# Kernel tuning notes

Measured on AMD Instinct MI355X. Metric: run time of the kernel, lower is better.

The kernel has to match this reference:

```python
import jax, jax.numpy as jnp
import numpy as np

NUM_HEADS = 16


def setup_inputs() -> dict:
    key = jax.random.key(0)
    ks = jax.random.split(key, 6)
    B, N, L, C = 2, 1024, 4096, 1024
    x_obj = jax.random.normal(ks[0], (B, N, C), dtype=jnp.float32)
    x_ctx = jax.random.normal(ks[1], (B, L, C), dtype=jnp.float32)
    s = 1.0 / np.sqrt(C)
    Wq = jax.random.normal(ks[2], (C, C), dtype=jnp.float32) * s
    Wkv = jax.random.normal(ks[3], (C, 2 * C), dtype=jnp.float32) * s
    Wproj = jax.random.normal(ks[4], (C, C), dtype=jnp.float32) * s
    bproj = jax.random.normal(ks[5], (C,), dtype=jnp.float32) * 0.01
    return {"x_obj": x_obj, "x_ctx": x_ctx, "Wq": Wq, "Wkv": Wkv,
            "Wproj": Wproj, "bproj": bproj}


def _split_heads(t, H):
    # [B, T, C] -> [B, H, T, d]
    B, T, C = t.shape
    return t.reshape(B, T, H, C // H).transpose(0, 2, 1, 3)


def reference(x_obj, x_ctx, Wq, Wkv, Wproj, bproj):
    B, N, C = x_obj.shape
    H = NUM_HEADS
    d = C // H
    scale = d ** -0.5

    q = _split_heads(x_obj @ Wq, H)                      # [B,H,N,d]

    kv_o = x_obj @ Wkv                                   # [B,N,2C] -> (2,H,d) split
    k_obj = _split_heads(kv_o[..., :C], H)               # [B,H,N,d]
    v_obj = _split_heads(kv_o[..., C:], H)

    kv_c = x_ctx @ Wkv                                   # [B,L,2C]
    k_ctx = _split_heads(kv_c[..., :C], H)               # [B,H,L,d]
    v_ctx = _split_heads(kv_c[..., C:], H)

    k = jnp.concatenate([k_obj, k_ctx], axis=2)          # [B,H,N+L,d]
    v = jnp.concatenate([v_obj, v_ctx], axis=2)

    attn = jnp.einsum('bhnd,bhmd->bhnm', q, k) * scale   # [B,H,N,N+L]
    attn = jax.nn.softmax(attn, axis=-1)
    out = jnp.einsum('bhnm,bhmd->bhnd', attn, v)         # [B,H,N,d]
    out = out.transpose(0, 2, 1, 3).reshape(B, N, C)
    return out @ Wproj + bproj
```

## Files before the change

### kernel.cpp

```cpp
#include <hip/hip_runtime.h>
#include <stdint.h>

typedef unsigned short u16;
typedef unsigned int   u32;
typedef __attribute__((ext_vector_type(8))) short bf16x8;
typedef __attribute__((ext_vector_type(4))) float f32x4;

__device__ __forceinline__ u16 f2bf(float f) {
    union { float f; u32 u; } v; v.f = f;
    return (u16)((v.u + 0x7FFFu + ((v.u >> 16) & 1u)) >> 16);
}
__device__ __forceinline__ float bf2f(u16 h) {
    union { u32 u; float f; } v; v.u = ((u32)h) << 16; return v.f;
}
__device__ __forceinline__ u32 fbits(float f) {
    union { float f; u32 u; } v; v.f = f; return v.u;
}

__device__ __forceinline__ void async16(const u16* g, u16* l) {
    typedef __attribute__((address_space(1))) const u32 gq;
    typedef __attribute__((address_space(3))) u32 lq;
    __builtin_amdgcn_global_load_lds((gq*)g, (lq*)l, 16, 0, 0);
}

__global__ void cvt_all_k(const float* __restrict__ xo, const float* __restrict__ xc,
                          u16* __restrict__ Xc,
                          const float* __restrict__ Wq, const float* __restrict__ Wkv,
                          const float* __restrict__ Wp,
                          u16* __restrict__ Wqt, u16* __restrict__ Wkt,
                          u16* __restrict__ Wpt)
{
    __shared__ __align__(16) u16 Ts[64][72];
    int id = blockIdx.x, t = threadIdx.x;
    if (id < 10240) {
        int row = id, cid = t * 4;
        int b = row >= 5120, s = row - b * 5120;
        const float* src = (s < 1024)
            ? xo + ((size_t)(b * 1024 + s)) * 1024 + cid
            : xc + ((size_t)(b * 4096 + s - 1024)) * 1024 + cid;
        float4 f = *(const float4*)src;
        union { u16 a[4]; uint2 v; } p;
        p.a[0]=f2bf(f.x); p.a[1]=f2bf(f.y); p.a[2]=f2bf(f.z); p.a[3]=f2bf(f.w);
        *(uint2*)(Xc + (size_t)row * 1024 + cid) = p.v;
        return;
    }
    int wid = id - 10240;
    const float* W; u16* Wt; int N, tile;
    if (wid < 256)      { W = Wq;  Wt = Wqt; N = 1024; tile = wid; }
    else if (wid < 768) { W = Wkv; Wt = Wkt; N = 2048; tile = wid - 256; }
    else                { W = Wp;  Wt = Wpt; N = 1024; tile = wid - 768; }
    int nt = N >> 6;
    int n0 = (tile % nt) * 64, k0 = (tile / nt) * 64;
    int lr = t >> 2, lc = (t & 3) * 16;
    const float* src = W + (size_t)(k0 + lr) * N + n0 + lc;
    union { u16 a[8]; uint4 v; } p0, p1;
    float4 f0 = *(const float4*)(src),      f1 = *(const float4*)(src + 4);
    float4 f2 = *(const float4*)(src + 8),  f3 = *(const float4*)(src + 12);
    p0.a[0]=f2bf(f0.x); p0.a[1]=f2bf(f0.y); p0.a[2]=f2bf(f0.z); p0.a[3]=f2bf(f0.w);
    p0.a[4]=f2bf(f1.x); p0.a[5]=f2bf(f1.y); p0.a[6]=f2bf(f1.z); p0.a[7]=f2bf(f1.w);
    p1.a[0]=f2bf(f2.x); p1.a[1]=f2bf(f2.y); p1.a[2]=f2bf(f2.z); p1.a[3]=f2bf(f2.w);
    p1.a[4]=f2bf(f3.x); p1.a[5]=f2bf(f3.y); p1.a[6]=f2bf(f3.z); p1.a[7]=f2bf(f3.w);
    *(uint4*)&Ts[lr][lc]     = p0.v;
    *(uint4*)&Ts[lr][lc + 8] = p1.v;
    __syncthreads();
    union { u16 a[8]; uint4 v; } q0, q1;
#pragma unroll
    for (int j = 0; j < 8; ++j) q0.a[j] = Ts[lc + j][lr];
#pragma unroll
    for (int j = 0; j < 8; ++j) q1.a[j] = Ts[lc + 8 + j][lr];
    u16* dst = Wt + (size_t)(n0 + lr) * 1024 + k0 + lc;
    *(uint4*)dst       = q0.v;
    *(uint4*)(dst + 8) = q1.v;
}

__global__ __launch_bounds__(256, 2)
void gemm_qkv(const u16* __restrict__ A, const u16* __restrict__ Wqt,
              const u16* __restrict__ Wkt, u16* __restrict__ q,
              u16* __restrict__ Kh, u16* __restrict__ Vh)
{
    __shared__ __align__(16) u16 smem[17408];
    u16* As = smem;
    u16* Bs = smem + 4096;

    const int t = threadIdx.x, w = t >> 6;
    const int lane = t & 63, quad = lane >> 4, l16 = lane & 15;
    const int id = blockIdx.x;
    const bool qm = id >= 1280;
    int m0, n0; const u16* Bt;
    if (qm) { int t2 = id - 1280; m0 = (t2 >> 3) * 128; n0 = (t2 & 7) * 128; Bt = Wqt; }
    else    { m0 = (id >> 4) * 128; n0 = (id & 15) * 128; Bt = Wkt; }
    const int wr = (w >> 1) * 64, wc = (w & 1) * 64;

    const int sr0 = w * 32 + (lane >> 2), sr1 = sr0 + 16;
    const int cg  = (lane & 3) ^ ((lane >> 4) & 3);
    u16* abase = As + w * 1024;
    u16* bbase = Bs + w * 1024;

    const u16 *ar0, *ar1;
    {
        int g0 = m0 + sr0, g1 = m0 + sr1;
        if (qm) {
            ar0 = A + ((size_t)(g0 >> 10) * 5120 + (g0 & 1023)) * 1024;
            ar1 = A + ((size_t)(g1 >> 10) * 5120 + (g1 & 1023)) * 1024;
        } else {
            ar0 = A + (size_t)g0 * 1024;
            ar1 = A + (size_t)g1 * 1024;
        }
        ar0 += cg * 8; ar1 += cg * 8;
    }
    const u16* br0 = Bt + (size_t)(n0 + sr0) * 1024 + cg * 8;
    const u16* br1 = Bt + (size_t)(n0 + sr1) * 1024 + cg * 8;

    f32x4 acc[4][4] = {};
    const int sel = (quad ^ (l16 >> 2)) * 8;

    for (int k0 = 0; k0 < 1024; k0 += 32) {
        async16(ar0 + k0, abase);
        async16(ar1 + k0, abase + 512);
        async16(br0 + k0, bbase);
        async16(br1 + k0, bbase + 512);
        __syncthreads();

        bf16x8 av[4], bv[4];
#pragma unroll
        for (int i = 0; i < 4; ++i)
            av[i] = *(const bf16x8*)&As[(wr + i * 16 + l16) * 32 + sel];
#pragma unroll
        for (int j = 0; j < 4; ++j)
            bv[j] = *(const bf16x8*)&Bs[(wc + j * 16 + l16) * 32 + sel];
#pragma unroll
        for (int i = 0; i < 4; ++i)
#pragma unroll
            for (int j = 0; j < 4; ++j)
                acc[i][j] = __builtin_amdgcn_mfma_f32_16x16x32_bf16(av[i], bv[j], acc[i][j], 0, 0, 0);
        __syncthreads();
    }

    if (qm) {
        const float SC = 0.180336880f;
#pragma unroll
        for (int j = 0; j < 4; ++j) {
            int col = n0 + wc + j * 16 + l16;
#pragma unroll
            for (int i = 0; i < 4; ++i) {
                int rowb = m0 + wr + i * 16 + quad * 4;
#pragma unroll
                for (int r = 0; r < 4; ++r)
                    q[(size_t)(rowb + r) * 1024 + col] = f2bf(acc[i][j][r] * SC);
            }
        }
        return;
    }
    int b = m0 >= 5120;
    int keyb = m0 - b * 5120;
    if (n0 < 1024) {
#pragma unroll
        for (int j = 0; j < 4; ++j) {
            int col = n0 + wc + j * 16 + l16;
#pragma unroll
            for (int i = 0; i < 4; ++i) {
                int rowb = m0 + wr + i * 16 + quad * 4;
                int key = rowb - b * 5120;
                int bh = b * 16 + (col >> 6), d = col & 63;
                u16* dst = Kh + ((size_t)bh * 5120 + key) * 64 + d;
#pragma unroll
                for (int r = 0; r < 4; ++r) dst[r * 64] = f2bf(acc[i][j][r]);
            }
        }
    } else {
        u16* T = smem;
#pragma unroll
        for (int j = 0; j < 4; ++j) {
            int d2 = wc + j * 16 + l16;
#pragma unroll
            for (int i = 0; i < 4; ++i) {
                int kl = wr + i * 16 + quad * 4;
                union { u16 a[4]; uint2 v; } pk;
#pragma unroll
                for (int r = 0; r < 4; ++r) pk.a[r] = f2bf(acc[i][j][r]);
                *(uint2*)&T[d2 * 136 + kl] = pk.v;
            }
        }
        __syncthreads();
        int hb = (n0 - 1024) >> 6;
#pragma unroll
        for (int p = 0; p < 8; ++p) {
            int idx = p * 256 + t;
            int d2 = idx >> 4, k0c = (idx & 15) * 8;
            uint4 vv = *(const uint4*)&T[d2 * 136 + k0c];
            int bh = b * 16 + hb + (d2 >> 6), d = d2 & 63;
            *(uint4*)(Vh + ((size_t)bh * 64 + d) * 5120 + keyb + k0c) = vv;
        }
    }
}

__global__ __launch_bounds__(256, 2)
void gemm_proj(const u16* __restrict__ A, const u16* __restrict__ Bt,
               const float* __restrict__ bias, float* __restrict__ Cf)
{
    __shared__ __align__(16) u16 As[128 * 32];
    __shared__ __align__(16) u16 Bs[64 * 32];

    const int t = threadIdx.x, w = t >> 6;
    const int lane = t & 63, quad = lane >> 4, l16 = lane & 15;
    const int m0 = blockIdx.y * 128, n0 = blockIdx.x * 64;
    const int wr = w * 32;

    const int sr0 = w * 32 + (lane >> 2), sr1 = sr0 + 16;
    const int cg  = (lane & 3) ^ ((lane >> 4) & 3);
    u16* abase = As + w * 1024;
    u16* bbase = Bs + w * 512;

    const u16* ar0 = A + (size_t)(m0 + sr0) * 1024 + cg * 8;
    const u16* ar1 = A + (size_t)(m0 + sr1) * 1024 + cg * 8;
    const u16* br0 = Bt + (size_t)(n0 + w * 16 + (lane >> 2)) * 1024 + cg * 8;

    f32x4 acc[2][4] = {};
    const int sel = (quad ^ (l16 >> 2)) * 8;

    for (int k0 = 0; k0 < 1024; k0 += 32) {
        async16(ar0 + k0, abase);
        async16(ar1 + k0, abase + 512);
        async16(br0 + k0, bbase);
        __syncthreads();

        bf16x8 av[2], bv[4];
#pragma unroll
        for (int i = 0; i < 2; ++i)
            av[i] = *(const bf16x8*)&As[(wr + i * 16 + l16) * 32 + sel];
#pragma unroll
        for (int j = 0; j < 4; ++j)
            bv[j] = *(const bf16x8*)&Bs[(j * 16 + l16) * 32 + sel];
#pragma unroll
        for (int i = 0; i < 2; ++i)
#pragma unroll
            for (int j = 0; j < 4; ++j)
                acc[i][j] = __builtin_amdgcn_mfma_f32_16x16x32_bf16(av[i], bv[j], acc[i][j], 0, 0, 0);
        __syncthreads();
    }

#pragma unroll
    for (int j = 0; j < 4; ++j) {
        int col = n0 + j * 16 + l16;
        float bvl = bias[col];
#pragma unroll
        for (int i = 0; i < 2; ++i) {
            int rowb = m0 + wr + i * 16 + quad * 4;
#pragma unroll
            for (int r = 0; r < 4; ++r)
                Cf[(size_t)(rowb + r) * 1024 + col] = acc[i][j][r] + bvl;
        }
    }
}

__global__ __launch_bounds__(256, 4)
void attn_k(const u16* __restrict__ Q, const u16* __restrict__ Kh,
            const u16* __restrict__ Vh, u16* __restrict__ Op,
            float* __restrict__ Lp)
{
    __shared__ __align__(16) u16 Ks[2][4096];
    __shared__ __align__(16) u16 Vt[4096];
    __shared__ __align__(16) u16 Ps[4096];

    const int tid  = threadIdx.x;
    const int wave = tid >> 6, lane = tid & 63;
    const int quad = lane >> 4, l16 = lane & 15;
    const int bx = blockIdx.x;
    const int x   = bx & 7;
    const int seq = bx >> 3;
    const int qt  = seq & 7;
    const int kg  = seq >> 3;
    const int g   = x + 8 * kg;
    const int part = g >> 5;
    const int bh   = g & 31;
    const int h = bh & 15, b = bh >> 4;

    const int qrow0 = b * 1024 + qt * 128 + wave * 32;
    const u16* qbase = Q + (size_t)qrow0 * 1024 + h * 64;

    bf16x8 aq[2][2];
#pragma unroll
    for (int rt = 0; rt < 2; ++rt) {
        aq[rt][0] = *(const bf16x8*)(qbase + (size_t)(rt * 16 + l16) * 1024 +      quad * 8);
        aq[rt][1] = *(const bf16x8*)(qbase + (size_t)(rt * 16 + l16) * 1024 + 32 + quad * 8);
    }

    union { u32 u[4]; bf16x8 v; } onesf;
#pragma unroll
    for (int i = 0; i < 4; ++i) onesf.u[i] = 0x3F803F80u;

    f32x4 o[2][4] = {};
    f32x4 lacc[2] = {};

    const u16* kbase = Kh + (size_t)bh * 5120 * 64;
    const u16* vbase = Vh + (size_t)bh * 64 * 5120;
    const int srow = tid >> 2;
    const int scg  = (tid & 3) * 2;
    const int m7   = srow & 7;
    const int l7   = l16 & 7;
    u16* vdst0 = Vt + srow * 64 + ((scg ^ m7) * 8);
    u16* vdst1 = Vt + srow * 64 + (((scg + 1) ^ m7) * 8);
    u16* psw   = Ps + wave * 1024;
    const int m_beg = part * 1024;

    const int keyA = tid >> 3;
    const int chA  = (tid & 7) ^ (keyA & 7);
    const u16* kga = kbase + (size_t)(m_beg + keyA) * 64 + chA * 8;
    u16* klds = &Ks[0][0] + wave * 512;

    const u16* vptr = vbase + (size_t)srow * 5120 + m_beg + (tid & 3) * 4;

    async16(kga,        klds);
    async16(kga + 2048, klds + 2048);
    uint2 vg0 = *(const uint2*)(vptr);
    uint2 vg1 = *(const uint2*)(vptr + 16);
    uint2 vg2 = *(const uint2*)(vptr + 32);
    uint2 vg3 = *(const uint2*)(vptr + 48);

    for (int c = 0; c < 16; ++c) {
        {
            uint4 o0, o1;
            o0.x = __builtin_amdgcn_perm(vg1.x, vg0.x, 0x05040100u);
            o0.y = __builtin_amdgcn_perm(vg3.x, vg2.x, 0x05040100u);
            o0.z = __builtin_amdgcn_perm(vg1.x, vg0.x, 0x07060302u);
            o0.w = __builtin_amdgcn_perm(vg3.x, vg2.x, 0x07060302u);
            o1.x = __builtin_amdgcn_perm(vg1.y, vg0.y, 0x05040100u);
            o1.y = __builtin_amdgcn_perm(vg3.y, vg2.y, 0x05040100u);
            o1.z = __builtin_amdgcn_perm(vg1.y, vg0.y, 0x07060302u);
            o1.w = __builtin_amdgcn_perm(vg3.y, vg2.y, 0x07060302u);
            *(uint4*)vdst0 = o0;
            *(uint4*)vdst1 = o1;
        }
        __syncthreads();

        if (c < 15) {
            const u16* ka = kga + (size_t)(c + 1) * 4096;
            u16* kd = &Ks[0][0] + ((c + 1) & 1) * 4096 + wave * 512;
            async16(ka,        kd);
            async16(ka + 2048, kd + 2048);
            const u16* vp = vptr + (c + 1) * 64;
            vg0 = *(const uint2*)(vp);
            vg1 = *(const uint2*)(vp + 16);
            vg2 = *(const uint2*)(vp + 32);
            vg3 = *(const uint2*)(vp + 48);
        }

        const u16* KsC = &Ks[0][0] + (c & 1) * 4096;
        f32x4 s[2][4] = {};
        __builtin_amdgcn_s_setprio(1);
#pragma unroll
        for (int nt = 0; nt < 4; ++nt) {
            const u16* krow = KsC + (nt * 16 + l16) * 64;
            bf16x8 kb0 = *(const bf16x8*)(krow + ((quad     ^ l7) * 8));
            bf16x8 kb1 = *(const bf16x8*)(krow + (((4+quad) ^ l7) * 8));
#pragma unroll
            for (int rt = 0; rt < 2; ++rt) {
                s[rt][nt] = __builtin_amdgcn_mfma_f32_16x16x32_bf16(aq[rt][0], kb0, s[rt][nt], 0, 0, 0);
                s[rt][nt] = __builtin_amdgcn_mfma_f32_16x16x32_bf16(aq[rt][1], kb1, s[rt][nt], 0, 0, 0);
            }
        }
        __builtin_amdgcn_s_setprio(0);

#pragma unroll
        for (int rt = 0; rt < 2; ++rt) {
#pragma unroll
            for (int r = 0; r < 4; ++r) {
                float e0 = exp2f(s[rt][0][r]);
                float e1 = exp2f(s[rt][1][r]);
                float e2 = exp2f(s[rt][2][r]);
                float e3 = exp2f(s[rt][3][r]);
                uint2 pw;
                pw.x = __builtin_amdgcn_perm(fbits(e1), fbits(e0), 0x07060302u);
                pw.y = __builtin_amdgcn_perm(fbits(e3), fbits(e2), 0x07060302u);
                int qr = quad * 4 + r;
                *(uint2*)(psw + qr * 64 +
                          (((l16 >> 1) ^ (qr & 7)) * 8) + (l16 & 1) * 4) = pw;
            }

            asm volatile("s_waitcnt lgkmcnt(0)" ::: "memory");

            const u16* prow = psw + l16 * 64;
            bf16x8 pf0 = *(const bf16x8*)(prow + ((quad     ^ l7) * 8));
            bf16x8 pf1 = *(const bf16x8*)(prow + (((4+quad) ^ l7) * 8));

            __builtin_amdgcn_s_setprio(1);
            lacc[rt] = __builtin_amdgcn_mfma_f32_16x16x32_bf16(pf0, onesf.v, lacc[rt], 0, 0, 0);
            lacc[rt] = __builtin_amdgcn_mfma_f32_16x16x32_bf16(pf1, onesf.v, lacc[rt], 0, 0, 0);
#pragma unroll
            for (int dt = 0; dt < 4; ++dt) {
                const u16* vrow = Vt + (dt * 16 + l16) * 64;
                bf16x8 v0 = *(const bf16x8*)(vrow + ((quad     ^ l7) * 8));
                bf16x8 v1 = *(const bf16x8*)(vrow + (((4+quad) ^ l7) * 8));
                o[rt][dt] = __builtin_amdgcn_mfma_f32_16x16x32_bf16(pf0, v0, o[rt][dt], 0, 0, 0);
                o[rt][dt] = __builtin_amdgcn_mfma_f32_16x16x32_bf16(pf1, v1, o[rt][dt], 0, 0, 0);
            }
            __builtin_amdgcn_s_setprio(0);
        }
        __syncthreads();
    }

    const int Rb = bh * 1024 + qt * 128 + wave * 32;
    u16* obase = Op + ((size_t)part << 21);
#pragma unroll
    for (int rt = 0; rt < 2; ++rt)
#pragma unroll
        for (int dt = 0; dt < 4; ++dt)
#pragma unroll
            for (int r = 0; r < 4; ++r) {
                int R = Rb + rt * 16 + quad * 4 + r;
                obase[(size_t)R * 64 + dt * 16 + l16] = f2bf(o[rt][dt][r]);
            }
    if (l16 == 0) {
#pragma unroll
        for (int rt = 0; rt < 2; ++rt)
#pragma unroll
            for (int r = 0; r < 4; ++r)
                Lp[part * 32768 + Rb + rt * 16 + quad * 4 + r] = lacc[rt][r];
    }
}

__global__ void comb_k(const u16* __restrict__ Op, const float* __restrict__ Lp,
                       u16* __restrict__ ao)
{
    int t = blockIdx.x * 256 + threadIdx.x;
    int R = t >> 4, dg = (t & 15) * 4;
    float l = Lp[R] + Lp[32768 + R] + Lp[65536 + R] + Lp[98304 + R] + Lp[131072 + R];
    float a[4] = {0.f, 0.f, 0.f, 0.f};
#pragma unroll
    for (int p = 0; p < 5; ++p) {
        union { u16 a[4]; uint2 v; } w;
        w.v = *(const uint2*)(Op + ((size_t)p << 21) + (size_t)R * 64 + dg);
#pragma unroll
        for (int j = 0; j < 4; ++j) a[j] += bf2f(w.a[j]);
    }
    float inv = 1.f / l;
    int bh = R >> 10, n = R & 1023, b = bh >> 4, h = bh & 15;
    union { u16 a[4]; uint2 v; } out;
#pragma unroll
    for (int j = 0; j < 4; ++j) out.a[j] = f2bf(a[j] * inv);
    *(uint2*)(ao + (size_t)(b * 1024 + n) * 1024 + h * 64 + dg) = out.v;
}

extern "C" void kernel_launch(void* const* d_in, const int* in_sizes, int n_in,
                              void* d_out, int out_size, void* d_ws, size_t ws_size,
                              hipStream_t stream)
{
    const float* x_obj = (const float*)d_in[0];
    const float* x_ctx = (const float*)d_in[1];
    const float* Wq    = (const float*)d_in[2];
    const float* Wkv   = (const float*)d_in[3];
    const float* Wproj = (const float*)d_in[4];
    const float* bproj = (const float*)d_in[5];
    float* out = (float*)d_out;

    u16* Xc  = (u16*)d_ws;
    u16* ao  = Xc;
    u16* Op  = Xc + (size_t)2097152;
    u16* Wqt = Xc  + (size_t)10485760;
    u16* Wkt = Wqt + (size_t)1048576;
    u16* Wpt = Wkt + (size_t)2097152;
    u16* q   = Wpt + (size_t)1048576;
    u16* Kh  = q   + (size_t)2097152;
    u16* Vh  = Kh  + (size_t)10485760;
    float* Lp = (float*)(Wkt + (size_t)1048576);

    dim3 blk(256);
    cvt_all_k<<<dim3(11264), blk, 0, stream>>>(x_obj, x_ctx, Xc,
                                               Wq, Wkv, Wproj, Wqt, Wkt, Wpt);
    gemm_qkv<<<dim3(1408), blk, 0, stream>>>(Xc, Wqt, Wkt, q, Kh, Vh);
    attn_k<<<dim3(1280), blk, 0, stream>>>(q, Kh, Vh, Op, Lp);
    comb_k<<<dim3(2048), blk, 0, stream>>>(Op, Lp, ao);
    gemm_proj<<<dim3(16, 16), blk, 0, stream>>>(ao, Wpt, bproj, out);
}
```

Before: 258.4 us.

## Halve attention tiles to 64 query rows and 32-key chunks, doubling grid

```diff
diff --git a/kernel.cpp b/kernel.cpp
--- a/kernel.cpp
+++ b/kernel.cpp
@@ -258,9 +258,9 @@
             const u16* __restrict__ Vh, u16* __restrict__ Op,
             float* __restrict__ Lp)
 {
-    __shared__ __align__(16) u16 Ks[2][4096];
-    __shared__ __align__(16) u16 Vt[4096];
-    __shared__ __align__(16) u16 Ps[4096];
+    __shared__ __align__(16) u16 Ks[2][2048];
+    __shared__ __align__(16) u16 Vt[2048];
+    __shared__ __align__(16) u16 Ps[2048];
 
     const int tid  = threadIdx.x;
     const int wave = tid >> 6, lane = tid & 63;
@@ -268,39 +268,31 @@
     const int bx = blockIdx.x;
     const int x   = bx & 7;
     const int seq = bx >> 3;
-    const int qt  = seq & 7;
-    const int kg  = seq >> 3;
+    const int qt  = seq & 15;
+    const int kg  = seq >> 4;
     const int g   = x + 8 * kg;
     const int part = g >> 5;
     const int bh   = g & 31;
     const int h = bh & 15, b = bh >> 4;
 
-    const int qrow0 = b * 1024 + qt * 128 + wave * 32;
+    const int qrow0 = b * 1024 + qt * 64 + wave * 16;
     const u16* qbase = Q + (size_t)qrow0 * 1024 + h * 64;
 
-    bf16x8 aq[2][2];
-#pragma unroll
-    for (int rt = 0; rt < 2; ++rt) {
-        aq[rt][0] = *(const bf16x8*)(qbase + (size_t)(rt * 16 + l16) * 1024 +      quad * 8);
-        aq[rt][1] = *(const bf16x8*)(qbase + (size_t)(rt * 16 + l16) * 1024 + 32 + quad * 8);
-    }
+    bf16x8 aq0 = *(const bf16x8*)(qbase + (size_t)l16 * 1024 +      quad * 8);
+    bf16x8 aq1 = *(const bf16x8*)(qbase + (size_t)l16 * 1024 + 32 + quad * 8);
 
     union { u32 u[4]; bf16x8 v; } onesf;
 #pragma unroll
     for (int i = 0; i < 4; ++i) onesf.u[i] = 0x3F803F80u;
 
-    f32x4 o[2][4] = {};
-    f32x4 lacc[2] = {};
+    f32x4 o[4] = {};
+    f32x4 lacc = {};
 
     const u16* kbase = Kh + (size_t)bh * 5120 * 64;
     const u16* vbase = Vh + (size_t)bh * 64 * 5120;
-    const int srow = tid >> 2;
-    const int scg  = (tid & 3) * 2;
-    const int m7   = srow & 7;
-    const int l7   = l16 & 7;
-    u16* vdst0 = Vt + srow * 64 + ((scg ^ m7) * 8);
-    u16* vdst1 = Vt + srow * 64 + (((scg + 1) ^ m7) * 8);
-    u16* psw   = Ps + wave * 1024;
+    const int l7  = l16 & 7;
+    const int sw4 = (l16 >> 1) & 3;
+    u16* psw = Ps + wave * 512;
     const int m_beg = part * 1024;
 
     const int keyA = tid >> 3;
@@ -308,114 +300,88 @@
     const u16* kga = kbase + (size_t)(m_beg + keyA) * 64 + chA * 8;
     u16* klds = &Ks[0][0] + wave * 512;
 
-    const u16* vptr = vbase + (size_t)srow * 5120 + m_beg + (tid & 3) * 4;
-
-    async16(kga,        klds);
-    async16(kga + 2048, klds + 2048);
-    uint2 vg0 = *(const uint2*)(vptr);
-    uint2 vg1 = *(const uint2*)(vptr + 16);
-    uint2 vg2 = *(const uint2*)(vptr + 32);
-    uint2 vg3 = *(const uint2*)(vptr + 48);
-
-    for (int c = 0; c < 16; ++c) {
+    const int vd = tid >> 2, vc = tid & 3;
+    const u16* vptr = vbase + (size_t)vd * 5120 + m_beg + vc * 4;
+    u16* vdst = Vt + vd * 32 + ((vc ^ ((vd >> 1) & 3)) << 3);
+
+    async16(kga, klds);
+    uint2 g0 = *(const uint2*)(vptr);
+    uint2 g1 = *(const uint2*)(vptr + 16);
+
+    for (int c = 0; c < 32; ++c) {
         {
-            uint4 o0, o1;
-            o0.x = __builtin_amdgcn_perm(vg1.x, vg0.x, 0x05040100u);
-            o0.y = __builtin_amdgcn_perm(vg3.x, vg2.x, 0x05040100u);
-            o0.z = __builtin_amdgcn_perm(vg1.x, vg0.x, 0x07060302u);
-            o0.w = __builtin_amdgcn_perm(vg3.x, vg2.x, 0x07060302u);
-            o1.x = __builtin_amdgcn_perm(vg1.y, vg0.y, 0x05040100u);
-            o1.y = __builtin_amdgcn_perm(vg3.y, vg2.y, 0x05040100u);
-            o1.z = __builtin_amdgcn_perm(vg1.y, vg0.y, 0x07060302u);
-            o1.w = __builtin_amdgcn_perm(vg3.y, vg2.y, 0x07060302u);
-            *(uint4*)vdst0 = o0;
-            *(uint4*)vdst1 = o1;
-        }
-        __syncthreads();
-
-        if (c < 15) {
-            const u16* ka = kga + (size_t)(c + 1) * 4096;
-            u16* kd = &Ks[0][0] + ((c + 1) & 1) * 4096 + wave * 512;
-            async16(ka,        kd);
-            async16(ka + 2048, kd + 2048);
-            const u16* vp = vptr + (c + 1) * 64;
-            vg0 = *(const uint2*)(vp);
-            vg1 = *(const uint2*)(vp + 16);
-            vg2 = *(const uint2*)(vp + 32);
-            vg3 = *(const uint2*)(vp + 48);
-        }
-
-        const u16* KsC = &Ks[0][0] + (c & 1) * 4096;
-        f32x4 s[2][4] = {};
+            uint4 ov;
+            ov.x = __builtin_amdgcn_perm(g1.x, g0.x, 0x05040100u);
+            ov.y = __builtin_amdgcn_perm(g1.x, g0.x, 0x07060302u);
+            ov.z = __builtin_amdgcn_perm(g1.y, g0.y, 0x05040100u);
+            ov.w = __builtin_amdgcn_perm(g1.y, g0.y, 0x07060302u);
+            *(uint4*)vdst = ov;
+        }
+        __syncthreads();
+
+        if (c < 31) {
+            async16(kga + (size_t)(c + 1) * 2048,
+                    &Ks[0][0] + ((c + 1) & 1) * 2048 + wave * 512);
+            const u16* vp = vptr + (c + 1) * 32;
+            g0 = *(const uint2*)(vp);
+            g1 = *(const uint2*)(vp + 16);
+        }
+
+        const u16* KsC = &Ks[0][0] + (c & 1) * 2048;
+        f32x4 s0 = {}, s1 = {};
         __builtin_amdgcn_s_setprio(1);
-#pragma unroll
-        for (int nt = 0; nt < 4; ++nt) {
-            const u16* krow = KsC + (nt * 16 + l16) * 64;
-            bf16x8 kb0 = *(const bf16x8*)(krow + ((quad     ^ l7) * 8));
-            bf16x8 kb1 = *(const bf16x8*)(krow + (((4+quad) ^ l7) * 8));
-#pragma unroll
-            for (int rt = 0; rt < 2; ++rt) {
-                s[rt][nt] = __builtin_amdgcn_mfma_f32_16x16x32_bf16(aq[rt][0], kb0, s[rt][nt], 0, 0, 0);
-                s[rt][nt] = __builtin_amdgcn_mfma_f32_16x16x32_bf16(aq[rt][1], kb1, s[rt][nt], 0, 0, 0);
-            }
+        {
+            const u16* kr0 = KsC + l16 * 64;
+            bf16x8 a0 = *(const bf16x8*)(kr0 + ((quad       ^ l7) << 3));
+            bf16x8 a1 = *(const bf16x8*)(kr0 + (((4 + quad) ^ l7) << 3));
+            s0 = __builtin_amdgcn_mfma_f32_16x16x32_bf16(aq0, a0, s0, 0, 0, 0);
+            s0 = __builtin_amdgcn_mfma_f32_16x16x32_bf16(aq1, a1, s0, 0, 0, 0);
+            const u16* kr1 = KsC + (16 + l16) * 64;
+            bf16x8 b0 = *(const bf16x8*)(kr1 + ((quad       ^ l7) << 3));
+            bf16x8 b1 = *(const bf16x8*)(kr1 + (((4 + quad) ^ l7) << 3));
+            s1 = __builtin_amdgcn_mfma_f32_16x16x32_bf16(aq0, b0, s1, 0, 0, 0);
+            s1 = __builtin_amdgcn_mfma_f32_16x16x32_bf16(aq1, b1, s1, 0, 0, 0);
         }
         __builtin_amdgcn_s_setprio(0);
 
 #pragma unroll
-        for (int rt = 0; rt < 2; ++rt) {
-#pragma unroll
-            for (int r = 0; r < 4; ++r) {
-                float e0 = exp2f(s[rt][0][r]);
-                float e1 = exp2f(s[rt][1][r]);
-                float e2 = exp2f(s[rt][2][r]);
-                float e3 = exp2f(s[rt][3][r]);
-                uint2 pw;
-                pw.x = __builtin_amdgcn_perm(fbits(e1), fbits(e0), 0x07060302u);
-                pw.y = __builtin_amdgcn_perm(fbits(e3), fbits(e2), 0x07060302u);
-                int qr = quad * 4 + r;
-                *(uint2*)(psw + qr * 64 +
-                          (((l16 >> 1) ^ (qr & 7)) * 8) + (l16 & 1) * 4) = pw;
-            }
-
-            asm volatile("s_waitcnt lgkmcnt(0)" ::: "memory");
-
-            const u16* prow = psw + l16 * 64;
-            bf16x8 pf0 = *(const bf16x8*)(prow + ((quad     ^ l7) * 8));
-            bf16x8 pf1 = *(const bf16x8*)(prow + (((4+quad) ^ l7) * 8));
-
-            __builtin_amdgcn_s_setprio(1);
-            lacc[rt] = __builtin_amdgcn_mfma_f32_16x16x32_bf16(pf0, onesf.v, lacc[rt], 0, 0, 0);
-            lacc[rt] = __builtin_amdgcn_mfma_f32_16x16x32_bf16(pf1, onesf.v, lacc[rt], 0, 0, 0);
-#pragma unroll
-            for (int dt = 0; dt < 4; ++dt) {
-                const u16* vrow = Vt + (dt * 16 + l16) * 64;
-                bf16x8 v0 = *(const bf16x8*)(vrow + ((quad     ^ l7) * 8));
-                bf16x8 v1 = *(const bf16x8*)(vrow + (((4+quad) ^ l7) * 8));
-                o[rt][dt] = __builtin_amdgcn_mfma_f32_16x16x32_bf16(pf0, v0, o[rt][dt], 0, 0, 0);
-                o[rt][dt] = __builtin_amdgcn_mfma_f32_16x16x32_bf16(pf1, v1, o[rt][dt], 0, 0, 0);
-            }
-            __builtin_amdgcn_s_setprio(0);
-        }
-        __syncthreads();
-    }
-
-    const int Rb = bh * 1024 + qt * 128 + wave * 32;
+        for (int r = 0; r < 4; ++r) {
+            float e0 = exp2f(s0[r]);
+            float e1 = exp2f(s1[r]);
+            u32 pw = __builtin_amdgcn_perm(fbits(e1), fbits(e0), 0x07060302u);
+            int qr = quad * 4 + r;
+            *(u32*)(psw + qr * 32 + (((l16 >> 2) ^ ((qr >> 1) & 3)) << 3)
+                        + ((l16 & 3) << 1)) = pw;
+        }
+
+        asm volatile("s_waitcnt lgkmcnt(0)" ::: "memory");
+
+        bf16x8 pf = *(const bf16x8*)(psw + l16 * 32 + ((quad ^ sw4) << 3));
+
+        __builtin_amdgcn_s_setprio(1);
+        lacc = __builtin_amdgcn_mfma_f32_16x16x32_bf16(pf, onesf.v, lacc, 0, 0, 0);
+#pragma unroll
+        for (int dt = 0; dt < 4; ++dt) {
+            bf16x8 vf = *(const bf16x8*)(Vt + (dt * 16 + l16) * 32 + ((quad ^ sw4) << 3));
+            o[dt] = __builtin_amdgcn_mfma_f32_16x16x32_bf16(pf, vf, o[dt], 0, 0, 0);
+        }
+        __builtin_amdgcn_s_setprio(0);
+        __syncthreads();
+    }
+
+    const int Rb = bh * 1024 + qt * 64 + wave * 16;
     u16* obase = Op + ((size_t)part << 21);
 #pragma unroll
-    for (int rt = 0; rt < 2; ++rt)
-#pragma unroll
-        for (int dt = 0; dt < 4; ++dt)
-#pragma unroll
-            for (int r = 0; r < 4; ++r) {
-                int R = Rb + rt * 16 + quad * 4 + r;
-                obase[(size_t)R * 64 + dt * 16 + l16] = f2bf(o[rt][dt][r]);
-            }
+    for (int dt = 0; dt < 4; ++dt)
+#pragma unroll
+        for (int r = 0; r < 4; ++r) {
+            int R = Rb + quad * 4 + r;
+            obase[(size_t)R * 64 + dt * 16 + l16] = f2bf(o[dt][r]);
+        }
     if (l16 == 0) {
 #pragma unroll
-        for (int rt = 0; rt < 2; ++rt)
-#pragma unroll
-            for (int r = 0; r < 4; ++r)
-                Lp[part * 32768 + Rb + rt * 16 + quad * 4 + r] = lacc[rt][r];
+        for (int r = 0; r < 4; ++r)
+            Lp[part * 32768 + Rb + quad * 4 + r] = lacc[r];
     }
 }
 
@@ -468,7 +434,7 @@
     cvt_all_k<<<dim3(11264), blk, 0, stream>>>(x_obj, x_ctx, Xc,
                                                Wq, Wkv, Wproj, Wqt, Wkt, Wpt);
     gemm_qkv<<<dim3(1408), blk, 0, stream>>>(Xc, Wqt, Wkt, q, Kh, Vh);
-    attn_k<<<dim3(1280), blk, 0, stream>>>(q, Kh, Vh, Op, Lp);
+    attn_k<<<dim3(2560), blk, 0, stream>>>(q, Kh, Vh, Op, Lp);
     comb_k<<<dim3(2048), blk, 0, stream>>>(Op, Lp, ao);
     gemm_proj<<<dim3(16, 16), blk, 0, stream>>>(ao, Wpt, bproj, out);
 }
```

Result: no change. 258.9 us (+0.2%).

## Double-buffer V tile via async LDS loads and drop second barrier

Applied to the files above, without the earlier changes.

```diff
diff --git a/kernel.cpp b/kernel.cpp
--- a/kernel.cpp
+++ b/kernel.cpp
@@ -259,7 +259,7 @@
             float* __restrict__ Lp)
 {
     __shared__ __align__(16) u16 Ks[2][4096];
-    __shared__ __align__(16) u16 Vt[4096];
+    __shared__ __align__(16) u16 Vt[2][4096];
     __shared__ __align__(16) u16 Ps[4096];
 
     const int tid  = threadIdx.x;
@@ -294,58 +294,41 @@
 
     const u16* kbase = Kh + (size_t)bh * 5120 * 64;
     const u16* vbase = Vh + (size_t)bh * 64 * 5120;
-    const int srow = tid >> 2;
-    const int scg  = (tid & 3) * 2;
-    const int m7   = srow & 7;
-    const int l7   = l16 & 7;
-    u16* vdst0 = Vt + srow * 64 + ((scg ^ m7) * 8);
-    u16* vdst1 = Vt + srow * 64 + (((scg + 1) ^ m7) * 8);
-    u16* psw   = Ps + wave * 1024;
+    const int l7 = l16 & 7;
+    u16* psw = Ps + wave * 1024;
     const int m_beg = part * 1024;
 
-    const int keyA = tid >> 3;
-    const int chA  = (tid & 7) ^ (keyA & 7);
-    const u16* kga = kbase + (size_t)(m_beg + keyA) * 64 + chA * 8;
-    u16* klds = &Ks[0][0] + wave * 512;
-
-    const u16* vptr = vbase + (size_t)srow * 5120 + m_beg + (tid & 3) * 4;
-
-    async16(kga,        klds);
-    async16(kga + 2048, klds + 2048);
-    uint2 vg0 = *(const uint2*)(vptr);
-    uint2 vg1 = *(const uint2*)(vptr + 16);
-    uint2 vg2 = *(const uint2*)(vptr + 32);
-    uint2 vg3 = *(const uint2*)(vptr + 48);
+    const int r1 = tid >> 3;
+    const int sl = tid & 7;
+    const int xs = sl ^ (r1 & 7);
+    const u16* kga = kbase + (size_t)(m_beg + 2 * r1) * 64 + xs * 8;
+    const u16* vga = vbase + (size_t)r1 * 5120 + m_beg + xs * 8;
+    u16* kldsw = &Ks[0][0] + wave * 512;
+    u16* vldsw = &Vt[0][0] + wave * 512;
+
+    async16(kga,              kldsw);
+    async16(kga + 64,         kldsw + 2048);
+    async16(vga,              vldsw);
+    async16(vga + 32 * 5120,  vldsw + 2048);
 
     for (int c = 0; c < 16; ++c) {
-        {
-            uint4 o0, o1;
-            o0.x = __builtin_amdgcn_perm(vg1.x, vg0.x, 0x05040100u);
-            o0.y = __builtin_amdgcn_perm(vg3.x, vg2.x, 0x05040100u);
-            o0.z = __builtin_amdgcn_perm(vg1.x, vg0.x, 0x07060302u);
-            o0.w = __builtin_amdgcn_perm(vg3.x, vg2.x, 0x07060302u);
-            o1.x = __builtin_amdgcn_perm(vg1.y, vg0.y, 0x05040100u);
-            o1.y = __builtin_amdgcn_perm(vg3.y, vg2.y, 0x05040100u);
-            o1.z = __builtin_amdgcn_perm(vg1.y, vg0.y, 0x07060302u);
-            o1.w = __builtin_amdgcn_perm(vg3.y, vg2.y, 0x07060302u);
-            *(uint4*)vdst0 = o0;
-            *(uint4*)vdst1 = o1;
-        }
         __syncthreads();
 
         if (c < 15) {
+            const int nb = (c + 1) & 1;
             const u16* ka = kga + (size_t)(c + 1) * 4096;
-            u16* kd = &Ks[0][0] + ((c + 1) & 1) * 4096 + wave * 512;
-            async16(ka,        kd);
-            async16(ka + 2048, kd + 2048);
-            const u16* vp = vptr + (c + 1) * 64;
-            vg0 = *(const uint2*)(vp);
-            vg1 = *(const uint2*)(vp + 16);
-            vg2 = *(const uint2*)(vp + 32);
-            vg3 = *(const uint2*)(vp + 48);
-        }
-
-        const u16* KsC = &Ks[0][0] + (c & 1) * 4096;
+            const u16* va = vga + (c + 1) * 64;
+            u16* kd = &Ks[nb][0] + wave * 512;
+            u16* vd = &Vt[nb][0] + wave * 512;
+            async16(ka,             kd);
+            async16(ka + 64,        kd + 2048);
+            async16(va,             vd);
+            async16(va + 32 * 5120, vd + 2048);
+        }
+
+        const u16* KsC = &Ks[c & 1][0];
+        const u16* VtC = &Vt[c & 1][0];
+
         f32x4 s[2][4] = {};
         __builtin_amdgcn_s_setprio(1);
 #pragma unroll
@@ -369,12 +352,12 @@
                 float e1 = exp2f(s[rt][1][r]);
                 float e2 = exp2f(s[rt][2][r]);
                 float e3 = exp2f(s[rt][3][r]);
-                uint2 pw;
-                pw.x = __builtin_amdgcn_perm(fbits(e1), fbits(e0), 0x07060302u);
-                pw.y = __builtin_amdgcn_perm(fbits(e3), fbits(e2), 0x07060302u);
+                u32 pwx = __builtin_amdgcn_perm(fbits(e2), fbits(e0), 0x07060302u);
+                u32 pwy = __builtin_amdgcn_perm(fbits(e3), fbits(e1), 0x07060302u);
                 int qr = quad * 4 + r;
-                *(uint2*)(psw + qr * 64 +
-                          (((l16 >> 1) ^ (qr & 7)) * 8) + (l16 & 1) * 4) = pw;
+                u16* prow = psw + qr * 64;
+                *(u32*)(prow + ((( (l16 >> 2)    ) ^ (qr & 7)) * 8) + (l16 & 3) * 2) = pwx;
+                *(u32*)(prow + ((( (l16 >> 2) + 4) ^ (qr & 7)) * 8) + (l16 & 3) * 2) = pwy;
             }
 
             asm volatile("s_waitcnt lgkmcnt(0)" ::: "memory");
@@ -388,7 +371,7 @@
             lacc[rt] = __builtin_amdgcn_mfma_f32_16x16x32_bf16(pf1, onesf.v, lacc[rt], 0, 0, 0);
 #pragma unroll
             for (int dt = 0; dt < 4; ++dt) {
-                const u16* vrow = Vt + (dt * 16 + l16) * 64;
+                const u16* vrow = VtC + (dt * 16 + l16) * 64;
                 bf16x8 v0 = *(const bf16x8*)(vrow + ((quad     ^ l7) * 8));
                 bf16x8 v1 = *(const bf16x8*)(vrow + (((4+quad) ^ l7) * 8));
                 o[rt][dt] = __builtin_amdgcn_mfma_f32_16x16x32_bf16(pf0, v0, o[rt][dt], 0, 0, 0);
@@ -396,7 +379,6 @@
             }
             __builtin_amdgcn_s_setprio(0);
         }
-        __syncthreads();
     }
 
     const int Rb = bh * 1024 + qt * 128 + wave * 32;
```

Result: faster. 247.5 us (-4.2%).
